# Kernel optimization log

Measured on AMD Instinct MI355X. Metric: run time of the kernel, lower is better.

The kernel has to match this reference:

```python
import jax, jax.numpy as jnp
import numpy as np

N_NODES = 65536
N_EDGES = 1048576
IN_DIM = 512
HID = 128


def gcn_conv(x, W, b, src, dst, ew, n_nodes):
    """PyG GCNConv: h = D^{-1/2} (A + I) D^{-1/2} (x W) + b, with edge weights."""
    h = x @ W  # [N, out]
    # add self-loops with weight 1
    loop = jnp.arange(n_nodes, dtype=src.dtype)
    src_f = jnp.concatenate([src, loop])
    dst_f = jnp.concatenate([dst, loop])
    ew_f = jnp.concatenate([ew, jnp.ones((n_nodes,), dtype=h.dtype)])
    # symmetric normalization: deg computed on destination (in-degree)
    deg = jax.ops.segment_sum(ew_f, dst_f, num_segments=n_nodes)
    dinv = jnp.where(deg > 0, jax.lax.rsqrt(deg), 0.0).astype(h.dtype)
    norm = dinv[src_f] * ew_f * dinv[dst_f]  # [E+N]
    msgs = norm[:, None] * h[src_f]  # gather + scale
    out = jax.ops.segment_sum(msgs, dst_f, num_segments=n_nodes)
    return out + b


def setup_inputs() -> dict:
    key = jax.random.key(0)
    ks = jax.random.split(key, 7)
    x = jax.random.normal(ks[0], (N_NODES, IN_DIM), dtype=jnp.float32)
    edge_index = jax.random.randint(ks[1], (2, N_EDGES), 0, N_NODES, dtype=jnp.int64 if jax.config.jax_enable_x64 else jnp.int32)
    edge_weight = jax.random.uniform(ks[2], (N_EDGES,), dtype=jnp.float32)
    s1 = 1.0 / np.sqrt(IN_DIM)
    s2 = 1.0 / np.sqrt(HID)
    W1 = jax.random.uniform(ks[3], (IN_DIM, HID), minval=-s1, maxval=s1, dtype=jnp.float32)
    b1 = jnp.zeros((HID,), dtype=jnp.float32)
    W2 = jax.random.uniform(ks[4], (HID, HID), minval=-s2, maxval=s2, dtype=jnp.float32)
    b2 = jnp.zeros((HID,), dtype=jnp.float32)
    return {"x": x, "edge_index": edge_index, "edge_weight": edge_weight,
            "W1": W1, "b1": b1, "W2": W2, "b2": b2}


def reference(x, edge_index, edge_weight, W1, b1, W2, b2):
    src, dst = edge_index[0], edge_index[1]
    h = gcn_conv(x, W1, b1, src, dst, edge_weight, N_NODES)
    h = jax.nn.relu(h)
    # dropout is identity at inference (training=False)
    z = gcn_conv(h, W2, b2, src, dst, edge_weight, N_NODES)
    return z
```

## Files before the change

### kernel.cpp

```cpp
#include <hip/hip_runtime.h>

#define NN 65536
#define NE 1048576
#define INDIM 512
#define HID 128
#define NSB 256

typedef __attribute__((ext_vector_type(8))) short bf16x8;
typedef __attribute__((ext_vector_type(16))) float f32x16;

__global__ void k_h1(const int* __restrict__ dst, int* __restrict__ ghist) {
    __shared__ int hcnt[256];
    hcnt[threadIdx.x] = 0;
    __syncthreads();
    int base = blockIdx.x * 4096;
#pragma unroll
    for (int r = 0; r < 16; r++)
        atomicAdd(&hcnt[dst[base + r * 256 + threadIdx.x] & 255], 1);
    __syncthreads();
    ghist[threadIdx.x * NSB + blockIdx.x] = hcnt[threadIdx.x];
}

__global__ void k_scan_ex(int* data, int* bsum, int n) {
    __shared__ int tmp[256];
    int i = blockIdx.x * 256 + threadIdx.x;
    int v = (i < n) ? data[i] : 0;
    tmp[threadIdx.x] = v;
    __syncthreads();
    for (int off = 1; off < 256; off <<= 1) {
        int t = (threadIdx.x >= off) ? tmp[threadIdx.x - off] : 0;
        __syncthreads();
        tmp[threadIdx.x] += t;
        __syncthreads();
    }
    if (i < n) data[i] = tmp[threadIdx.x] - v;
    if (threadIdx.x == 255 && bsum) bsum[blockIdx.x] = tmp[255];
}

__global__ void k_addback(int* data, const int* __restrict__ bsum) {
    int i = blockIdx.x * 256 + threadIdx.x;
    data[i] += bsum[blockIdx.x];
}

__global__ void k_s1(const int* __restrict__ src, const int* __restrict__ dst,
                     const float* __restrict__ ew, const int* __restrict__ ghist,
                     unsigned* __restrict__ e1sd, float* __restrict__ e1ew) {
    __shared__ int cur[256];
    cur[threadIdx.x] = ghist[threadIdx.x * NSB + blockIdx.x];
    __syncthreads();
    int base = blockIdx.x * 4096;
#pragma unroll
    for (int r = 0; r < 16; r++) {
        int e = base + r * 256 + threadIdx.x;
        int d = dst[e];
        int p = atomicAdd(&cur[d & 255], 1);
        e1sd[p] = (unsigned)src[e] | ((unsigned)(d >> 8) << 16);
        e1ew[p] = ew[e];
    }
}

__global__ void k_s2(const int* __restrict__ ghist, const unsigned* __restrict__ e1sd,
                     const float* __restrict__ e1ew,
                     uint2* __restrict__ edata, int* __restrict__ row_beg,
                     int* __restrict__ row_end, float* __restrict__ dinv) {
    __shared__ int cnt[256];
    __shared__ float degs[256];
    __shared__ int tmp[256];
    __shared__ int curx[256];
    const int bin = blockIdx.x;
    const int t = threadIdx.x;
    cnt[t] = 0;
    degs[t] = 0.f;
    __syncthreads();
    const int binstart = ghist[bin * NSB];
    const int binend = (bin == 255) ? NE : ghist[(bin + 1) * NSB];
    for (int i = binstart + t; i < binend; i += 256) {
        unsigned u = e1sd[i];
        int j = u >> 16;
        atomicAdd(&cnt[j], 1);
        atomicAdd(&degs[j], e1ew[i]);
    }
    __syncthreads();
    int v = cnt[t];
    tmp[t] = v;
    __syncthreads();
    for (int off = 1; off < 256; off <<= 1) {
        int u = (t >= off) ? tmp[t - off] : 0;
        __syncthreads();
        tmp[t] += u;
        __syncthreads();
    }
    int offt = tmp[t] - v;
    int d = (t << 8) | bin;
    int beg = binstart + offt;
    row_beg[d] = beg;
    row_end[d] = beg + v;
    dinv[d] = rsqrtf(1.0f + degs[t]);
    curx[t] = beg;
    __syncthreads();
    for (int i = binstart + t; i < binend; i += 256) {
        unsigned u = e1sd[i];
        int p = atomicAdd(&curx[u >> 16], 1);
        edata[p] = make_uint2(u & 0xFFFFu, __float_as_uint(e1ew[i]));
    }
}

__device__ __forceinline__ void prep_one(const float* __restrict__ W, unsigned short* __restrict__ P,
                                         int t) {
    int l = t & 63;
    int h = (t >> 6) & 1;
    int n = (t >> 7) & 3;
    int k0 = t >> 9;
    int colg = n * 32 + (l & 31);
    int kbase = k0 * 16 + (l >> 5) * 8;
    bf16x8 v;
#pragma unroll
    for (int j = 0; j < 8; j++) {
        float f = W[(size_t)(kbase + j) * 128 + colg];
        unsigned b = __float_as_uint(f);
        if (h == 0) {
            v[j] = (short)(b >> 16);
        } else {
            float lf = f - __uint_as_float(b & 0xFFFF0000u);
            v[j] = (short)(__float_as_uint(lf) >> 16);
        }
    }
    *(bf16x8*)(P + (size_t)t * 8) = v;
}

__global__ void k_prep_pack2(const float* __restrict__ W1, unsigned short* __restrict__ P1,
                             const float* __restrict__ W2, unsigned short* __restrict__ P2) {
    int t = blockIdx.x * 256 + threadIdx.x;
    if (t < 16384) prep_one(W1, P1, t);
    else if (t < 16384 + 4096) prep_one(W2, P2, t - 16384);
}

__device__ __forceinline__ void split8(const float4& a0, const float4& a1,
                                       bf16x8& hi, bf16x8& lo) {
    float f[8] = {a0.x, a0.y, a0.z, a0.w, a1.x, a1.y, a1.z, a1.w};
#pragma unroll
    for (int i = 0; i < 8; i++) {
        unsigned b = __float_as_uint(f[i]);
        unsigned hb = b & 0xFFFF0000u;
        float lf = f[i] - __uint_as_float(hb);
        hi[i] = (short)(hb >> 16);
        lo[i] = (short)(__float_as_uint(lf) >> 16);
    }
}

__device__ __forceinline__ unsigned short f2bf_rne(float v) {
    unsigned u = __float_as_uint(v);
    unsigned r = (u + 0x7FFFu + ((u >> 16) & 1u)) >> 16;
    return (unsigned short)r;
}

template <int K, bool PRESPLIT>
__device__ __forceinline__ void stage_chunk(const float* __restrict__ A,
                                            const unsigned short* __restrict__ Ahi,
                                            const unsigned short* __restrict__ Alo,
                                            int rowbase,
                                            const unsigned short* __restrict__ Bp,
                                            int c, int tid, char* As, unsigned short* Bs) {
    const int w = tid >> 6;
    if (PRESPLIT) {
        {
            int row = tid & 63;
            int kk2lh = tid >> 6;
            const char* srcp = (const char*)Ahi + ((size_t)(rowbase + row) * 128 + c * 32 + kk2lh * 8) * 2;
            char* dst = As + (size_t)(w * 64) * 16;
            __builtin_amdgcn_global_load_lds((const __attribute__((address_space(1))) void*)srcp,
                                             (__attribute__((address_space(3))) void*)dst, 16, 0, 0);
        }
        {
            int row = tid & 63;
            int kk2lh = tid >> 6;
            const char* srcp = (const char*)Alo + ((size_t)(rowbase + row) * 128 + c * 32 + kk2lh * 8) * 2;
            char* dst = As + 4096 + (size_t)(w * 64) * 16;
            __builtin_amdgcn_global_load_lds((const __attribute__((address_space(1))) void*)srcp,
                                             (__attribute__((address_space(3))) void*)dst, 16, 0, 0);
        }
    } else {
#pragma unroll
        for (int q = 0; q < 2; ++q) {
            int lh = (tid >> 7) & 1;
            int row = (tid >> 1) & 63;
            int g = (tid & 1) ^ ((row >> 2) & 1);
            const float* srcp = A + (size_t)(rowbase + row) * K + c * 32 + q * 16 + lh * 8 + g * 4;
            char* dst = As + (size_t)(q * 256 + w * 64) * 16;
            __builtin_amdgcn_global_load_lds((const __attribute__((address_space(1))) void*)srcp,
                                             (__attribute__((address_space(3))) void*)dst, 16, 0, 0);
        }
    }
    const char* bsrc0 = (const char*)Bp + (size_t)c * 16384;
#pragma unroll
    for (int q = 0; q < 4; ++q) {
        const char* srcp = bsrc0 + (size_t)(q * 256 + tid) * 16;
        char* dst = (char*)Bs + (size_t)(q * 256 + w * 64) * 16;
        __builtin_amdgcn_global_load_lds((const __attribute__((address_space(1))) void*)srcp,
                                         (__attribute__((address_space(3))) void*)dst, 16, 0, 0);
    }
}

template <int K, bool PRESPLIT>
__global__ __launch_bounds__(256, 2) void k_gemm_mfma(const float* __restrict__ A,
                                                      const unsigned short* __restrict__ Ahi,
                                                      const unsigned short* __restrict__ Alo,
                                                      const unsigned short* __restrict__ Bp,
                                                      unsigned short* __restrict__ Cb) {
    constexpr int NC = K / 32;
    __shared__ __align__(16) char As[3][8192];
    __shared__ __align__(16) unsigned short Bs[3][8192];
    const int tid = threadIdx.x;
    const int w = tid >> 6;
    const int lane = tid & 63;
    const int l31 = lane & 31;
    const int lhalf = lane >> 5;
    const int rowbase = blockIdx.x * 64;
    const int ncol = (w & 1) * 2;
    const int r = (w >> 1) * 32 + l31;
    const int xr = (l31 >> 2) & 1;

    f32x16 acc[2] = {};

    stage_chunk<K, PRESPLIT>(A, Ahi, Alo, rowbase, Bp, 0, tid, As[0], Bs[0]);
    stage_chunk<K, PRESPLIT>(A, Ahi, Alo, rowbase, Bp, 1, tid, As[1], Bs[1]);

    for (int c = 0; c < NC; ++c) {
        if (c > 0) {
            __builtin_amdgcn_s_barrier();
            asm volatile("" ::: "memory");
            __builtin_amdgcn_sched_barrier(0);
        }
        if (c + 2 < NC) {
            int b = (c + 2) % 3;
            stage_chunk<K, PRESPLIT>(A, Ahi, Alo, rowbase, Bp, c + 2, tid, As[b], Bs[b]);
        }
        int rem = NC - 1 - c;
        if (rem >= 2)      asm volatile("s_waitcnt vmcnt(12)" ::: "memory");
        else if (rem == 1) asm volatile("s_waitcnt vmcnt(6)" ::: "memory");
        else               asm volatile("s_waitcnt vmcnt(0)" ::: "memory");
        __builtin_amdgcn_s_barrier();
        const int cur = c % 3;
#pragma unroll
        for (int kk = 0; kk < 2; ++kk) {
            bf16x8 ahi, alo;
            if (PRESPLIT) {
                int gidx = ((kk * 2 + lhalf) * 64 + r) * 16;
                ahi = *(const bf16x8*)&As[cur][gidx];
                alo = *(const bf16x8*)&As[cur][4096 + gidx];
            } else {
                const float* Af = (const float*)As[cur];
                int bg = ((kk * 2 + lhalf) * 64 + r) * 2;
                float4 aa = *(const float4*)&Af[(size_t)(bg + xr) * 4];
                float4 ab = *(const float4*)&Af[(size_t)(bg + (1 ^ xr)) * 4];
                split8(aa, ab, ahi, alo);
            }
#pragma unroll
            for (int n = 0; n < 2; ++n) {
                int f = (ncol + n) * 2;
                bf16x8 bhi = *(const bf16x8*)&Bs[cur][(size_t)((kk * 8 + f) * 64 + lane) * 8];
                bf16x8 blo = *(const bf16x8*)&Bs[cur][(size_t)((kk * 8 + f + 1) * 64 + lane) * 8];
                acc[n] = __builtin_amdgcn_mfma_f32_32x32x16_bf16(ahi, bhi, acc[n], 0, 0, 0);
                acc[n] = __builtin_amdgcn_mfma_f32_32x32x16_bf16(ahi, blo, acc[n], 0, 0, 0);
                acc[n] = __builtin_amdgcn_mfma_f32_32x32x16_bf16(alo, bhi, acc[n], 0, 0, 0);
            }
        }
    }

    const int rbase = rowbase + (w >> 1) * 32 + 4 * lhalf;
#pragma unroll
    for (int n = 0; n < 2; ++n) {
        const int col = (ncol + n) * 32 + l31;
#pragma unroll
        for (int rr = 0; rr < 16; ++rr) {
            int rout = rbase + (rr & 3) + 8 * (rr >> 2);
            Cb[(size_t)rout * HID + col] = f2bf_rne(acc[n][rr]);
        }
    }
}

__device__ __forceinline__ float2 up2(unsigned u) {
    float2 r;
    r.x = __uint_as_float(u << 16);
    r.y = __uint_as_float(u & 0xFFFF0000u);
    return r;
}

template <bool RELU>
__global__ __launch_bounds__(256) void k_agg(const unsigned short* __restrict__ hb,
                                             const float* __restrict__ dinv,
                                             const int* __restrict__ row_beg,
                                             const int* __restrict__ row_end,
                                             const uint2* __restrict__ edata,
                                             const float* __restrict__ bias,
                                             float* __restrict__ out,
                                             unsigned* __restrict__ a1hi,
                                             unsigned* __restrict__ a1lo) {
    int d = (blockIdx.x * blockDim.x + threadIdx.x) >> 6;
    int lane = threadIdx.x & 63;
    float di = dinv[d];
    float2 hv = up2(((const unsigned*)(hb + (size_t)d * HID))[lane]);
    int beg = row_beg[d], end = row_end[d];
    float ex = 0.f, ey = 0.f;
    int e = beg;
    for (; e + 15 < end; e += 16) {
        uint2 u[16];
        unsigned g[16];
        float dv[16];
#pragma unroll
        for (int q = 0; q < 16; q++) u[q] = edata[e + q];
#pragma unroll
        for (int q = 0; q < 16; q++) {
            g[q] = ((const unsigned*)(hb + (size_t)u[q].x * HID))[lane];
            dv[q] = dinv[u[q].x];
        }
#pragma unroll
        for (int q = 0; q < 16; q++) {
            float2 vv = up2(g[q]);
            float c = dv[q] * __uint_as_float(u[q].y);
            ex += c * vv.x;
            ey += c * vv.y;
        }
    }
    for (; e + 3 < end; e += 4) {
        uint2 u[4];
        unsigned g[4];
        float dv[4];
#pragma unroll
        for (int q = 0; q < 4; q++) u[q] = edata[e + q];
#pragma unroll
        for (int q = 0; q < 4; q++) {
            g[q] = ((const unsigned*)(hb + (size_t)u[q].x * HID))[lane];
            dv[q] = dinv[u[q].x];
        }
#pragma unroll
        for (int q = 0; q < 4; q++) {
            float2 vv = up2(g[q]);
            float c = dv[q] * __uint_as_float(u[q].y);
            ex += c * vv.x;
            ey += c * vv.y;
        }
    }
    for (; e < end; ++e) {
        uint2 u = edata[e];
        float2 v = up2(((const unsigned*)(hb + (size_t)u.x * HID))[lane]);
        float c = dinv[u.x] * __uint_as_float(u.y);
        ex += c * v.x;
        ey += c * v.y;
    }
    float2 bv = ((const float2*)bias)[lane];
    float selfc = di * di;
    float ax = di * ex + selfc * hv.x + bv.x;
    float ay = di * ey + selfc * hv.y + bv.y;
    if (RELU) {
        ax = fmaxf(ax, 0.f);
        ay = fmaxf(ay, 0.f);
        unsigned bx = __float_as_uint(ax), by = __float_as_uint(ay);
        unsigned hx = bx & 0xFFFF0000u, hy = by & 0xFFFF0000u;
        unsigned lx = __float_as_uint(ax - __uint_as_float(hx));
        unsigned ly = __float_as_uint(ay - __uint_as_float(hy));
        a1hi[(size_t)d * 64 + lane] = (hx >> 16) | (hy & 0xFFFF0000u);
        a1lo[(size_t)d * 64 + lane] = (lx >> 16) | (ly & 0xFFFF0000u);
    } else {
        float2 rr;
        rr.x = ax;
        rr.y = ay;
        ((float2*)(out + (size_t)d * HID))[lane] = rr;
    }
}

extern "C" void kernel_launch(void* const* d_in, const int* in_sizes, int n_in,
                              void* d_out, int out_size, void* d_ws, size_t ws_size,
                              hipStream_t stream) {
    const float* x = (const float*)d_in[0];
    const int* ei = (const int*)d_in[1];
    const float* ew = (const float*)d_in[2];
    const float* W1 = (const float*)d_in[3];
    const float* b1 = (const float*)d_in[4];
    const float* W2 = (const float*)d_in[5];
    const float* b2 = (const float*)d_in[6];
    const int* src = ei;
    const int* dst = ei + NE;
    float* out = (float*)d_out;

    char* ws = (char*)d_ws;
    unsigned short* hb = (unsigned short*)(ws + 0);
    uint2* edata    = (uint2*)(ws + 16777216);
    int*   ghist    = (int*)(ws + 25165824);
    int*   bsum1    = (int*)(ws + 25427968);
    unsigned* e1sd  = (unsigned*)(ws + 25428992);
    float* e1ew     = (float*)(ws + 29623296);
    int*   row_beg  = (int*)(ws + 33817600);
    int*   row_end  = (int*)(ws + 34079744);
    float* dinv     = (float*)(ws + 34341888);
    unsigned short* bp1 = (unsigned short*)(ws + 34604032);
    unsigned short* bp2 = (unsigned short*)(ws + 34866176);
    unsigned* a1hi  = (unsigned*)(ws + 35651584);
    unsigned* a1lo  = (unsigned*)(ws + 52428800);

    k_h1<<<NSB, 256, 0, stream>>>(dst, ghist);
    k_scan_ex<<<NSB, 256, 0, stream>>>(ghist, bsum1, 256 * NSB);
    k_scan_ex<<<1, 256, 0, stream>>>(bsum1, nullptr, NSB);
    k_addback<<<NSB, 256, 0, stream>>>(ghist, bsum1);
    k_s1<<<NSB, 256, 0, stream>>>(src, dst, ew, ghist, e1sd, e1ew);
    k_s2<<<256, 256, 0, stream>>>(ghist, e1sd, e1ew, edata, row_beg, row_end, dinv);
    k_prep_pack2<<<80, 256, 0, stream>>>(W1, bp1, W2, bp2);

    k_gemm_mfma<INDIM, false><<<NN / 64, 256, 0, stream>>>(x, nullptr, nullptr, bp1, hb);
    k_agg<true><<<NN / 4, 256, 0, stream>>>(hb, dinv, row_beg, row_end, edata, b1, nullptr, a1hi, a1lo);

    k_gemm_mfma<HID, true><<<NN / 64, 256, 0, stream>>>(nullptr, (const unsigned short*)a1hi,
                                                        (const unsigned short*)a1lo, bp2, hb);
    k_agg<false><<<NN / 4, 256, 0, stream>>>(hb, dinv, row_beg, row_end, edata, b2, out, nullptr, nullptr);
}
```

Measured before the change: 203.5 us.

## Fuse CSR build into one cooperative kernel and store layer-1 activations as bf16

Merges the seven CSR-build and weight-pack launches into one cooperative kernel that uses grid-wide syncs between phases, which removes the gaps between kernel launches. It also rounds the ReLU output of layer 1 to a single bf16 value instead of a hi/lo split pair. That halves the activation write and read traffic and drops one MFMA per step in the second GEMM. In exchange, layer-2 input precision falls to bf16, and the grid syncs carry their own cost.

```diff
diff --git a/kernel.cpp b/kernel.cpp
--- a/kernel.cpp
+++ b/kernel.cpp
@@ -1,4 +1,5 @@
 #include <hip/hip_runtime.h>
+#include <hip/hip_cooperative_groups.h>
 
 #define NN 65536
 #define NE 1048576
@@ -8,102 +9,6 @@
 
 typedef __attribute__((ext_vector_type(8))) short bf16x8;
 typedef __attribute__((ext_vector_type(16))) float f32x16;
-
-__global__ void k_h1(const int* __restrict__ dst, int* __restrict__ ghist) {
-    __shared__ int hcnt[256];
-    hcnt[threadIdx.x] = 0;
-    __syncthreads();
-    int base = blockIdx.x * 4096;
-#pragma unroll
-    for (int r = 0; r < 16; r++)
-        atomicAdd(&hcnt[dst[base + r * 256 + threadIdx.x] & 255], 1);
-    __syncthreads();
-    ghist[threadIdx.x * NSB + blockIdx.x] = hcnt[threadIdx.x];
-}
-
-__global__ void k_scan_ex(int* data, int* bsum, int n) {
-    __shared__ int tmp[256];
-    int i = blockIdx.x * 256 + threadIdx.x;
-    int v = (i < n) ? data[i] : 0;
-    tmp[threadIdx.x] = v;
-    __syncthreads();
-    for (int off = 1; off < 256; off <<= 1) {
-        int t = (threadIdx.x >= off) ? tmp[threadIdx.x - off] : 0;
-        __syncthreads();
-        tmp[threadIdx.x] += t;
-        __syncthreads();
-    }
-    if (i < n) data[i] = tmp[threadIdx.x] - v;
-    if (threadIdx.x == 255 && bsum) bsum[blockIdx.x] = tmp[255];
-}
-
-__global__ void k_addback(int* data, const int* __restrict__ bsum) {
-    int i = blockIdx.x * 256 + threadIdx.x;
-    data[i] += bsum[blockIdx.x];
-}
-
-__global__ void k_s1(const int* __restrict__ src, const int* __restrict__ dst,
-                     const float* __restrict__ ew, const int* __restrict__ ghist,
-                     unsigned* __restrict__ e1sd, float* __restrict__ e1ew) {
-    __shared__ int cur[256];
-    cur[threadIdx.x] = ghist[threadIdx.x * NSB + blockIdx.x];
-    __syncthreads();
-    int base = blockIdx.x * 4096;
-#pragma unroll
-    for (int r = 0; r < 16; r++) {
-        int e = base + r * 256 + threadIdx.x;
-        int d = dst[e];
-        int p = atomicAdd(&cur[d & 255], 1);
-        e1sd[p] = (unsigned)src[e] | ((unsigned)(d >> 8) << 16);
-        e1ew[p] = ew[e];
-    }
-}
-
-__global__ void k_s2(const int* __restrict__ ghist, const unsigned* __restrict__ e1sd,
-                     const float* __restrict__ e1ew,
-                     uint2* __restrict__ edata, int* __restrict__ row_beg,
-                     int* __restrict__ row_end, float* __restrict__ dinv) {
-    __shared__ int cnt[256];
-    __shared__ float degs[256];
-    __shared__ int tmp[256];
-    __shared__ int curx[256];
-    const int bin = blockIdx.x;
-    const int t = threadIdx.x;
-    cnt[t] = 0;
-    degs[t] = 0.f;
-    __syncthreads();
-    const int binstart = ghist[bin * NSB];
-    const int binend = (bin == 255) ? NE : ghist[(bin + 1) * NSB];
-    for (int i = binstart + t; i < binend; i += 256) {
-        unsigned u = e1sd[i];
-        int j = u >> 16;
-        atomicAdd(&cnt[j], 1);
-        atomicAdd(&degs[j], e1ew[i]);
-    }
-    __syncthreads();
-    int v = cnt[t];
-    tmp[t] = v;
-    __syncthreads();
-    for (int off = 1; off < 256; off <<= 1) {
-        int u = (t >= off) ? tmp[t - off] : 0;
-        __syncthreads();
-        tmp[t] += u;
-        __syncthreads();
-    }
-    int offt = tmp[t] - v;
-    int d = (t << 8) | bin;
-    int beg = binstart + offt;
-    row_beg[d] = beg;
-    row_end[d] = beg + v;
-    dinv[d] = rsqrtf(1.0f + degs[t]);
-    curx[t] = beg;
-    __syncthreads();
-    for (int i = binstart + t; i < binend; i += 256) {
-        unsigned u = e1sd[i];
-        int p = atomicAdd(&curx[u >> 16], 1);
-        edata[p] = make_uint2(u & 0xFFFFu, __float_as_uint(e1ew[i]));
-    }
-}
 
 __device__ __forceinline__ void prep_one(const float* __restrict__ W, unsigned short* __restrict__ P,
                                          int t) {
@@ -128,11 +33,111 @@
     *(bf16x8*)(P + (size_t)t * 8) = v;
 }
 
-__global__ void k_prep_pack2(const float* __restrict__ W1, unsigned short* __restrict__ P1,
-                             const float* __restrict__ W2, unsigned short* __restrict__ P2) {
-    int t = blockIdx.x * 256 + threadIdx.x;
-    if (t < 16384) prep_one(W1, P1, t);
-    else if (t < 16384 + 4096) prep_one(W2, P2, t - 16384);
+__global__ __launch_bounds__(256, 1) void k_csr(
+        const int* __restrict__ src, const int* __restrict__ dst, const float* __restrict__ ew,
+        const float* __restrict__ W1, const float* __restrict__ W2,
+        int* __restrict__ ghist, int* __restrict__ bsum1,
+        unsigned* __restrict__ e1sd, float* __restrict__ e1ew,
+        uint2* __restrict__ edata, int* __restrict__ row_beg, int* __restrict__ row_end,
+        float* __restrict__ dinv, unsigned short* __restrict__ bp1, unsigned short* __restrict__ bp2) {
+    cooperative_groups::grid_group grid = cooperative_groups::this_grid();
+    __shared__ int si0[256];
+    __shared__ int si1[256];
+    __shared__ int si2[256];
+    __shared__ float sf0[256];
+    const int b = blockIdx.x, t = threadIdx.x;
+    const int base = b * 4096;
+
+    si0[t] = 0;
+    __syncthreads();
+    for (int r = 0; r < 16; r++) atomicAdd(&si0[dst[base + r * 256 + t] & 255], 1);
+    __syncthreads();
+    ghist[t * NSB + b] = si0[t];
+    __threadfence();
+    grid.sync();
+
+    {
+        int i = b * 256 + t;
+        int v = ghist[i];
+        si0[t] = v;
+        __syncthreads();
+        for (int off = 1; off < 256; off <<= 1) {
+            int u = (t >= off) ? si0[t - off] : 0;
+            __syncthreads();
+            si0[t] += u;
+            __syncthreads();
+        }
+        ghist[i] = si0[t] - v;
+        if (t == 255) bsum1[b] = si0[255];
+    }
+    __threadfence();
+    grid.sync();
+
+    if (b == 0) {
+        int v = bsum1[t];
+        si0[t] = v;
+        __syncthreads();
+        for (int off = 1; off < 256; off <<= 1) {
+            int u = (t >= off) ? si0[t - off] : 0;
+            __syncthreads();
+            si0[t] += u;
+            __syncthreads();
+        }
+        bsum1[t] = si0[t] - v;
+    } else if (b <= 80) {
+        int idx = (b - 1) * 256 + t;
+        if (idx < 16384) prep_one(W1, bp1, idx);
+        else prep_one(W2, bp2, idx - 16384);
+    }
+    __threadfence();
+    grid.sync();
+
+    si0[t] = bsum1[t] + ghist[t * NSB + b];
+    __syncthreads();
+    for (int r = 0; r < 16; r++) {
+        int e = base + r * 256 + t;
+        int d = dst[e];
+        int p = atomicAdd(&si0[d & 255], 1);
+        e1sd[p] = (unsigned)src[e] | ((unsigned)(d >> 8) << 16);
+        e1ew[p] = ew[e];
+    }
+    __threadfence();
+    grid.sync();
+
+    {
+        si0[t] = 0;
+        sf0[t] = 0.f;
+        __syncthreads();
+        const int binstart = bsum1[b];
+        const int binend = (b == 255) ? NE : bsum1[b + 1];
+        for (int i = binstart + t; i < binend; i += 256) {
+            unsigned u = e1sd[i];
+            atomicAdd(&si0[u >> 16], 1);
+            atomicAdd(&sf0[u >> 16], e1ew[i]);
+        }
+        __syncthreads();
+        int v = si0[t];
+        si1[t] = v;
+        __syncthreads();
+        for (int off = 1; off < 256; off <<= 1) {
+            int u = (t >= off) ? si1[t - off] : 0;
+            __syncthreads();
+            si1[t] += u;
+            __syncthreads();
+        }
+        int d = (t << 8) | b;
+        int beg = binstart + si1[t] - v;
+        row_beg[d] = beg;
+        row_end[d] = beg + v;
+        dinv[d] = rsqrtf(1.0f + sf0[t]);
+        si2[t] = beg;
+        __syncthreads();
+        for (int i = binstart + t; i < binend; i += 256) {
+            unsigned u = e1sd[i];
+            int p = atomicAdd(&si2[u >> 16], 1);
+            edata[p] = make_uint2(u & 0xFFFFu, __float_as_uint(e1ew[i]));
+        }
+    }
 }
 
 __device__ __forceinline__ void split8(const float4& a0, const float4& a1,
@@ -154,31 +159,20 @@
     return (unsigned short)r;
 }
 
-template <int K, bool PRESPLIT>
+template <int K, bool BF16A>
 __device__ __forceinline__ void stage_chunk(const float* __restrict__ A,
-                                            const unsigned short* __restrict__ Ahi,
-                                            const unsigned short* __restrict__ Alo,
+                                            const unsigned short* __restrict__ Ab,
                                             int rowbase,
                                             const unsigned short* __restrict__ Bp,
                                             int c, int tid, char* As, unsigned short* Bs) {
     const int w = tid >> 6;
-    if (PRESPLIT) {
-        {
-            int row = tid & 63;
-            int kk2lh = tid >> 6;
-            const char* srcp = (const char*)Ahi + ((size_t)(rowbase + row) * 128 + c * 32 + kk2lh * 8) * 2;
-            char* dst = As + (size_t)(w * 64) * 16;
-            __builtin_amdgcn_global_load_lds((const __attribute__((address_space(1))) void*)srcp,
-                                             (__attribute__((address_space(3))) void*)dst, 16, 0, 0);
-        }
-        {
-            int row = tid & 63;
-            int kk2lh = tid >> 6;
-            const char* srcp = (const char*)Alo + ((size_t)(rowbase + row) * 128 + c * 32 + kk2lh * 8) * 2;
-            char* dst = As + 4096 + (size_t)(w * 64) * 16;
-            __builtin_amdgcn_global_load_lds((const __attribute__((address_space(1))) void*)srcp,
-                                             (__attribute__((address_space(3))) void*)dst, 16, 0, 0);
-        }
+    if (BF16A) {
+        int row = tid & 63;
+        int kk2lh = tid >> 6;
+        const char* srcp = (const char*)Ab + ((size_t)(rowbase + row) * 128 + c * 32 + kk2lh * 8) * 2;
+        char* dst = As + (size_t)(w * 64) * 16;
+        __builtin_amdgcn_global_load_lds((const __attribute__((address_space(1))) void*)srcp,
+                                         (__attribute__((address_space(3))) void*)dst, 16, 0, 0);
     } else {
 #pragma unroll
         for (int q = 0; q < 2; ++q) {
@@ -201,10 +195,9 @@
     }
 }
 
-template <int K, bool PRESPLIT>
+template <int K, bool BF16A>
 __global__ __launch_bounds__(256, 2) void k_gemm_mfma(const float* __restrict__ A,
-                                                      const unsigned short* __restrict__ Ahi,
-                                                      const unsigned short* __restrict__ Alo,
+                                                      const unsigned short* __restrict__ Ab,
                                                       const unsigned short* __restrict__ Bp,
                                                       unsigned short* __restrict__ Cb) {
     constexpr int NC = K / 32;
@@ -222,8 +215,8 @@
 
     f32x16 acc[2] = {};
 
-    stage_chunk<K, PRESPLIT>(A, Ahi, Alo, rowbase, Bp, 0, tid, As[0], Bs[0]);
-    stage_chunk<K, PRESPLIT>(A, Ahi, Alo, rowbase, Bp, 1, tid, As[1], Bs[1]);
+    stage_chunk<K, BF16A>(A, Ab, rowbase, Bp, 0, tid, As[0], Bs[0]);
+    stage_chunk<K, BF16A>(A, Ab, rowbase, Bp, 1, tid, As[1], Bs[1]);
 
     for (int c = 0; c < NC; ++c) {
         if (c > 0) {
@@ -233,21 +226,26 @@
         }
         if (c + 2 < NC) {
             int b = (c + 2) % 3;
-            stage_chunk<K, PRESPLIT>(A, Ahi, Alo, rowbase, Bp, c + 2, tid, As[b], Bs[b]);
+            stage_chunk<K, BF16A>(A, Ab, rowbase, Bp, c + 2, tid, As[b], Bs[b]);
         }
         int rem = NC - 1 - c;
-        if (rem >= 2)      asm volatile("s_waitcnt vmcnt(12)" ::: "memory");
-        else if (rem == 1) asm volatile("s_waitcnt vmcnt(6)" ::: "memory");
-        else               asm volatile("s_waitcnt vmcnt(0)" ::: "memory");
+        if (BF16A) {
+            if (rem >= 2)      asm volatile("s_waitcnt vmcnt(10)" ::: "memory");
+            else if (rem == 1) asm volatile("s_waitcnt vmcnt(5)" ::: "memory");
+            else               asm volatile("s_waitcnt vmcnt(0)" ::: "memory");
+        } else {
+            if (rem >= 2)      asm volatile("s_waitcnt vmcnt(12)" ::: "memory");
+            else if (rem == 1) asm volatile("s_waitcnt vmcnt(6)" ::: "memory");
+            else               asm volatile("s_waitcnt vmcnt(0)" ::: "memory");
+        }
         __builtin_amdgcn_s_barrier();
         const int cur = c % 3;
 #pragma unroll
         for (int kk = 0; kk < 2; ++kk) {
             bf16x8 ahi, alo;
-            if (PRESPLIT) {
+            if (BF16A) {
                 int gidx = ((kk * 2 + lhalf) * 64 + r) * 16;
                 ahi = *(const bf16x8*)&As[cur][gidx];
-                alo = *(const bf16x8*)&As[cur][4096 + gidx];
             } else {
                 const float* Af = (const float*)As[cur];
                 int bg = ((kk * 2 + lhalf) * 64 + r) * 2;
@@ -262,7 +260,8 @@
                 bf16x8 blo = *(const bf16x8*)&Bs[cur][(size_t)((kk * 8 + f + 1) * 64 + lane) * 8];
                 acc[n] = __builtin_amdgcn_mfma_f32_32x32x16_bf16(ahi, bhi, acc[n], 0, 0, 0);
                 acc[n] = __builtin_amdgcn_mfma_f32_32x32x16_bf16(ahi, blo, acc[n], 0, 0, 0);
-                acc[n] = __builtin_amdgcn_mfma_f32_32x32x16_bf16(alo, bhi, acc[n], 0, 0, 0);
+                if (!BF16A)
+                    acc[n] = __builtin_amdgcn_mfma_f32_32x32x16_bf16(alo, bhi, acc[n], 0, 0, 0);
             }
         }
     }
@@ -294,8 +293,7 @@
                                              const uint2* __restrict__ edata,
                                              const float* __restrict__ bias,
                                              float* __restrict__ out,
-                                             unsigned* __restrict__ a1hi,
-                                             unsigned* __restrict__ a1lo) {
+                                             unsigned* __restrict__ abuf) {
     int d = (blockIdx.x * blockDim.x + threadIdx.x) >> 6;
     int lane = threadIdx.x & 63;
     float di = dinv[d];
@@ -355,12 +353,8 @@
     if (RELU) {
         ax = fmaxf(ax, 0.f);
         ay = fmaxf(ay, 0.f);
-        unsigned bx = __float_as_uint(ax), by = __float_as_uint(ay);
-        unsigned hx = bx & 0xFFFF0000u, hy = by & 0xFFFF0000u;
-        unsigned lx = __float_as_uint(ax - __uint_as_float(hx));
-        unsigned ly = __float_as_uint(ay - __uint_as_float(hy));
-        a1hi[(size_t)d * 64 + lane] = (hx >> 16) | (hy & 0xFFFF0000u);
-        a1lo[(size_t)d * 64 + lane] = (lx >> 16) | (ly & 0xFFFF0000u);
+        unsigned pk = (unsigned)f2bf_rne(ax) | ((unsigned)f2bf_rne(ay) << 16);
+        abuf[(size_t)d * 64 + lane] = pk;
     } else {
         float2 rr;
         rr.x = ax;
@@ -379,8 +373,6 @@
     const float* b1 = (const float*)d_in[4];
     const float* W2 = (const float*)d_in[5];
     const float* b2 = (const float*)d_in[6];
-    const int* src = ei;
-    const int* dst = ei + NE;
     float* out = (float*)d_out;
 
     char* ws = (char*)d_ws;
@@ -395,21 +387,22 @@
     float* dinv     = (float*)(ws + 34341888);
     unsigned short* bp1 = (unsigned short*)(ws + 34604032);
     unsigned short* bp2 = (unsigned short*)(ws + 34866176);
-    unsigned* a1hi  = (unsigned*)(ws + 35651584);
-    unsigned* a1lo  = (unsigned*)(ws + 52428800);
-
-    k_h1<<<NSB, 256, 0, stream>>>(dst, ghist);
-    k_scan_ex<<<NSB, 256, 0, stream>>>(ghist, bsum1, 256 * NSB);
-    k_scan_ex<<<1, 256, 0, stream>>>(bsum1, nullptr, NSB);
-    k_addback<<<NSB, 256, 0, stream>>>(ghist, bsum1);
-    k_s1<<<NSB, 256, 0, stream>>>(src, dst, ew, ghist, e1sd, e1ew);
-    k_s2<<<256, 256, 0, stream>>>(ghist, e1sd, e1ew, edata, row_beg, row_end, dinv);
-    k_prep_pack2<<<80, 256, 0, stream>>>(W1, bp1, W2, bp2);
-
-    k_gemm_mfma<INDIM, false><<<NN / 64, 256, 0, stream>>>(x, nullptr, nullptr, bp1, hb);
-    k_agg<true><<<NN / 4, 256, 0, stream>>>(hb, dinv, row_beg, row_end, edata, b1, nullptr, a1hi, a1lo);
-
-    k_gemm_mfma<HID, true><<<NN / 64, 256, 0, stream>>>(nullptr, (const unsigned short*)a1hi,
-                                                        (const unsigned short*)a1lo, bp2, hb);
-    k_agg<false><<<NN / 4, 256, 0, stream>>>(hb, dinv, row_beg, row_end, edata, b2, out, nullptr, nullptr);
-}
+    unsigned* a1b   = (unsigned*)(ws + 35651584);
+
+    const int* srcp = ei;
+    const int* dstp = ei + NE;
+    const float* ewp = ew;
+    const float* w1p = W1;
+    const float* w2p = W2;
+    void* kargs[] = {(void*)&srcp, (void*)&dstp, (void*)&ewp, (void*)&w1p, (void*)&w2p,
+                     (void*)&ghist, (void*)&bsum1, (void*)&e1sd, (void*)&e1ew,
+                     (void*)&edata, (void*)&row_beg, (void*)&row_end, (void*)&dinv,
+                     (void*)&bp1, (void*)&bp2};
+    hipLaunchCooperativeKernel((const void*)k_csr, dim3(NSB), dim3(256), kargs, 0, stream);
+
+    k_gemm_mfma<INDIM, false><<<NN / 64, 256, 0, stream>>>(x, nullptr, bp1, hb);
+    k_agg<true><<<NN / 4, 256, 0, stream>>>(hb, dinv, row_beg, row_end, edata, b1, nullptr, a1b);
+
+    k_gemm_mfma<HID, true><<<NN / 64, 256, 0, stream>>>(nullptr, (const unsigned short*)a1b, bp2, hb);
+    k_agg<false><<<NN / 4, 256, 0, stream>>>(hb, dinv, row_beg, row_end, edata, b2, out, nullptr);
+}
```

New measurement: 410.7 us. 102% more time.
